# Kernel tuning notes

Measured on AMD Instinct MI355X. Metric: run time of the kernel, lower is better.

## Reference

```python
import jax, jax.numpy as jnp
import numpy as np
from functools import partial

H = 768
E = 1536
B = 4
L = 4096

def layer_norm(x, g, b, eps=1e-5):
    mu = jnp.mean(x, axis=-1, keepdims=True)
    var = jnp.mean((x - mu) ** 2, axis=-1, keepdims=True)
    return (x - mu) * jax.lax.rsqrt(var + eps) * g + b

def l2_normalize(x, eps=1e-12):
    n = jnp.sqrt(jnp.sum(x * x, axis=-1, keepdims=True))
    return x / jnp.maximum(n, eps)

def dw_conv(x, w):
    # x: [B, L, E], w: [E, 1, 3] depthwise kernel (torch Conv1d groups=E layout)
    y = jax.lax.conv_general_dilated(
        x.transpose(0, 2, 1), w, window_strides=(1,), padding=[(1, 1)],
        dimension_numbers=('NCH', 'OIH', 'NCH'), feature_group_count=E)
    return y.transpose(0, 2, 1)

def setup_inputs() -> dict:
    key = jax.random.key(0)
    ks = jax.random.split(key, 12)
    d = {}
    d['x'] = jax.random.normal(ks[0], (B, L, H), jnp.float32)
    d['ln1_g'] = jnp.ones((H,), jnp.float32)
    d['ln1_b'] = jnp.zeros((H,), jnp.float32)
    d['ln2_g'] = jnp.ones((E,), jnp.float32)
    d['ln2_b'] = jnp.zeros((E,), jnp.float32)
    d['W_in'] = 0.02 * jax.random.normal(ks[1], (3 * E, H), jnp.float32)
    d['b_in'] = jnp.zeros((3 * E,), jnp.float32)
    d['W_beta'] = jnp.zeros((E, H), jnp.float32)  # torch init: constant 0
    d['b_beta'] = jnp.ones((E,), jnp.float32)     # torch init: constant 1
    d['W_out'] = 0.02 * jax.random.normal(ks[2], (H, E), jnp.float32)
    d['b_out'] = jnp.zeros((H,), jnp.float32)
    d['W1'] = 0.02 * jax.random.normal(ks[3], (4 * H, H), jnp.float32)
    d['b1'] = jnp.zeros((4 * H,), jnp.float32)
    d['W2'] = 0.02 * jax.random.normal(ks[4], (H, 4 * H), jnp.float32)
    d['b2'] = jnp.zeros((H,), jnp.float32)
    d['conv_w'] = jax.random.normal(ks[5], (E, 1, 3), jnp.float32) / jnp.sqrt(3.0)
    d['attn_scale'] = jnp.ones((1,), jnp.float32)
    return d

def reference(x, ln1_g, ln1_b, ln2_g, ln2_b, W_in, b_in, W_beta, b_beta,
              W_out, b_out, W1, b1, W2, b2, conv_w, attn_scale):
    shortcut = x
    xn = layer_norm(x, ln1_g, ln1_b)
    qkv = xn @ W_in.T + b_in
    q, k, v = jnp.split(qkv, 3, axis=-1)
    q = jax.nn.silu(q)
    k = jax.nn.silu(k)
    v = jax.nn.gelu(v, approximate=False)
    q = l2_normalize(q) + 0.1 * k
    k = l2_normalize(k) + 0.1 * q
    q = dw_conv(q, conv_w)
    k = dw_conv(k, conv_w)
    v = dw_conv(v, conv_w)
    beta = jax.nn.sigmoid(xn @ W_beta.T + b_beta) * 0.9 + 0.1
    # initial state is zero, so v_old = 0 and v_new = beta * v (same math as torch code)
    v_new = beta * v                                   # [B, L, E]
    state = jnp.einsum('ble,blf->bef', v_new, k)       # v_new^T @ k : [B, E, E]
    out = jnp.einsum('blf,bef->ble', q, state)         # q @ state^T
    out = out * attn_scale
    out = layer_norm(out, ln2_g, ln2_b)
    out = out @ W_out.T + b_out
    x = shortcut + out
    h = layer_norm(x, ln1_g, ln1_b)
    h = jax.nn.gelu(h @ W1.T + b1, approximate=False) @ W2.T + b2
    return x + h
```

## Files before the change

### kernel.cpp

```cpp
#include <hip/hip_runtime.h>
#include <hip/hip_bf16.h>
#include <cstdint>
#include <cstddef>

using bf16_t = __hip_bfloat16;
typedef __bf16 bf16x8 __attribute__((ext_vector_type(8)));
typedef __bf16 bf16x4 __attribute__((ext_vector_type(4)));
typedef float f32x4 __attribute__((ext_vector_type(4)));

#define DEVI static __device__ __forceinline__

DEVI float b2f(bf16_t v) { return __bfloat162float(v); }

DEVI float fsigmoid(float x) { return 1.0f / (1.0f + __expf(-x)); }
DEVI float fsilu(float x) { return x * fsigmoid(x); }

DEVI float ferf(float x) {
    const float ax = fabsf(x);
    const float t = 1.0f / fmaf(0.3275911f, ax, 1.0f);
    float p = fmaf(1.061405429f, t, -1.453152027f);
    p = fmaf(p, t, 1.421413741f);
    p = fmaf(p, t, -0.284496736f);
    p = fmaf(p, t, 0.254829592f);
    p = p * t * __expf(-ax * ax);
    return copysignf(1.0f - p, x);
}
DEVI float fgelu(float x) { return 0.5f * x * (1.0f + ferf(x * 0.70710678118654752440f)); }

DEVI void g2l16(const bf16_t* g, bf16_t* l) {
    __builtin_amdgcn_global_load_lds(
        (const __attribute__((address_space(1))) void*)g,
        (__attribute__((address_space(3))) void*)l,
        16, 0, 0);
}

DEVI f32x4 mfma16(bf16x8 a, bf16x8 b, f32x4 c) {
    return __builtin_amdgcn_mfma_f32_16x16x32_bf16(a, b, c, 0, 0, 0);
}

template<int ACT, bool RESID, bool OUTBF, bool QKVSPLIT>
__global__ __launch_bounds__(256) void gemm_nt(
    const bf16_t* __restrict__ A, const bf16_t* __restrict__ B,
    void* __restrict__ Cout, const float* __restrict__ bias,
    const float* __restrict__ resid,
    float* __restrict__ normq, float* __restrict__ normk,
    int M, int N, int K, long long sA, long long sB, long long sC)
{
    __shared__ bf16_t As[128 * 64];
    __shared__ bf16_t Bs[128 * 64];

    const int t  = threadIdx.x;
    const int w  = t >> 6;
    const int ln = t & 63;
    const long long bz = blockIdx.z;
    A += bz * sA;
    B += bz * sB;
    const long long cbase = QKVSPLIT ? 0 : bz * sC;

    const int m0 = blockIdx.y * 128;
    const int n0 = blockIdx.x * 128;
    const int wm = (w >> 1) * 64;
    const int wn = (w & 1) * 64;

    f32x4 acc[4][4] = {};

    const int sr = ln >> 3;
    const int sc = (ln & 7) ^ sr;
    const bf16_t* Ap = A + (size_t)(m0 + w * 32 + sr) * K + sc * 8;
    const bf16_t* Bp = B + (size_t)(n0 + w * 32 + sr) * K + sc * 8;
    bf16_t* ldsA = &As[(w * 32) * 64];
    bf16_t* ldsB = &Bs[(w * 32) * 64];

    const int fr = ln & 15;
    const int qd = ln >> 4;
    int roA[4], roB[4];
#pragma unroll
    for (int i = 0; i < 4; ++i) {
        roA[i] = (wm + i * 16 + fr) * 64;
        roB[i] = (wn + i * 16 + fr) * 64;
    }
    const int so0 = ((qd)     ^ (fr & 7)) * 8;
    const int so1 = ((4 + qd) ^ (fr & 7)) * 8;

    for (int k0 = 0; k0 < K; k0 += 64) {
#pragma unroll
        for (int i = 0; i < 4; ++i) {
            g2l16(Ap + (size_t)(i * 8) * K, ldsA + (i * 8) * 64);
            g2l16(Bp + (size_t)(i * 8) * K, ldsB + (i * 8) * 64);
        }
        Ap += 64; Bp += 64;
        __syncthreads();

        bf16x8 af[4], bfr[4];
#pragma unroll
        for (int i = 0; i < 4; ++i) {
            af[i]  = *(const bf16x8*)&As[roA[i] + so0];
            bfr[i] = *(const bf16x8*)&Bs[roB[i] + so0];
        }
#pragma unroll
        for (int mi = 0; mi < 4; ++mi)
#pragma unroll
            for (int ni = 0; ni < 4; ++ni)
                acc[mi][ni] = mfma16(bfr[ni], af[mi], acc[mi][ni]);
#pragma unroll
        for (int i = 0; i < 4; ++i) {
            af[i]  = *(const bf16x8*)&As[roA[i] + so1];
            bfr[i] = *(const bf16x8*)&Bs[roB[i] + so1];
        }
#pragma unroll
        for (int mi = 0; mi < 4; ++mi)
#pragma unroll
            for (int ni = 0; ni < 4; ++ni)
                acc[mi][ni] = mfma16(bfr[ni], af[mi], acc[mi][ni]);
        __syncthreads();
    }

    const int rb = qd * 4;
    const int seg = QKVSPLIT ? (n0 / 1536) : 0;
    f32x4 bias4[4];
#pragma unroll
    for (int ni = 0; ni < 4; ++ni) {
        f32x4 z = {};
        bias4[ni] = bias ? *(const f32x4*)&bias[n0 + wn + ni * 16 + rb] : z;
    }
#pragma unroll
    for (int mi = 0; mi < 4; ++mi) {
        const int row = m0 + wm + mi * 16 + fr;
        float s2 = 0.f;
#pragma unroll
        for (int ni = 0; ni < 4; ++ni) {
            const int col0 = n0 + wn + ni * 16 + rb;
            f32x4 v = acc[mi][ni] + bias4[ni];
            if constexpr (ACT == 1) {
#pragma unroll
                for (int r = 0; r < 4; ++r) v[r] = fgelu(v[r]);
            }
            if constexpr (ACT == 3) {
                if (seg <= 1) {
#pragma unroll
                    for (int r = 0; r < 4; ++r) v[r] = fsilu(v[r]);
                    s2 += v[0]*v[0] + v[1]*v[1] + v[2]*v[2] + v[3]*v[3];
                } else if (seg == 2) {
#pragma unroll
                    for (int r = 0; r < 4; ++r) v[r] = fgelu(v[r]);
                } else {
#pragma unroll
                    for (int r = 0; r < 4; ++r) v[r] = fsigmoid(v[r]) * 0.9f + 0.1f;
                }
            }
            long long off;
            if constexpr (QKVSPLIT) {
                off = (long long)seg * sC + (long long)row * 1536
                    + (col0 - seg * 1536);
            } else {
                off = cbase + (long long)row * N + col0;
            }
            if constexpr (RESID) v += *(const f32x4*)&resid[off];
            if constexpr (OUTBF) {
                bf16x4 o;
#pragma unroll
                for (int r = 0; r < 4; ++r) o[r] = (__bf16)v[r];
                *(bf16x4*)((bf16_t*)Cout + off) = o;
            } else {
                *(f32x4*)((float*)Cout + off) = v;
            }
        }
        if constexpr (ACT == 3) {
            if (seg <= 1) {
                s2 += __shfl_xor(s2, 16, 64);
                s2 += __shfl_xor(s2, 32, 64);
                if (qd == 0)
                    atomicAdd((seg == 0 ? normq : normk) + row, s2);
            }
        }
    }
}

template<int ACT, bool RESID, bool OUTBF, bool QKVSPLIT>
__global__ __launch_bounds__(512) void gemm256(
    const bf16_t* __restrict__ A, const bf16_t* __restrict__ B,
    void* __restrict__ Cout, const float* __restrict__ bias,
    const float* __restrict__ resid,
    float* __restrict__ normq, float* __restrict__ normk,
    int M, int N, int K, long long sA, long long sB, long long sC)
{
    __shared__ bf16_t As[2][256 * 64];
    __shared__ bf16_t Bs[2][256 * 64];

    const int t  = threadIdx.x;
    const int w  = t >> 6;
    const int ln = t & 63;
    const int wr = w >> 2;
    const int wc = w & 3;
    const long long bz = blockIdx.z;
    A += bz * sA;
    B += bz * sB;
    const long long cbase = QKVSPLIT ? 0 : bz * sC;

    const int m0 = blockIdx.y * 256;
    const int n0 = blockIdx.x * 256;

    const int sr = ln >> 3;
    const int scx = ((ln & 7) ^ sr) * 8;
    const bf16_t* gA[2];
    const bf16_t* gB[2];
    int lA[2], lB[2];
#pragma unroll
    for (int i = 0; i < 2; ++i) {
        const int b  = w * 2 + i;
        const int rA = ((b >> 3) << 7) + ((b & 7) << 3);
        const int rB = ((b >> 2) << 6) + ((b & 3) << 3);
        gA[i] = A + (size_t)(m0 + rA + sr) * K + scx;
        gB[i] = B + (size_t)(n0 + rB + sr) * K + scx;
        lA[i] = rA * 64;
        lB[i] = rB * 64;
    }
    const size_t K64 = (size_t)K * 64;
    const size_t K32 = (size_t)K * 32;
    const int NT = K >> 6;

    const int fr = ln & 15;
    const int qd = ln >> 4;
    const int ck0 = ((qd)     ^ (fr & 7)) * 8;
    const int ck1 = ((4 + qd) ^ (fr & 7)) * 8;
    int roA[8], roB[4];
#pragma unroll
    for (int mi = 0; mi < 8; ++mi) roA[mi] = (wr * 128 + mi * 16 + fr) * 64;
#pragma unroll
    for (int ni = 0; ni < 4; ++ni) roB[ni] = (wc * 64 + ni * 16 + fr) * 64;

    f32x4 acc[8][4] = {};

#define STAGE_A(dst, kc) do { \
    g2l16(gA[0] + (kc),       &(dst)[lA[0]]); \
    g2l16(gA[0] + K64 + (kc), &(dst)[lA[0] + 4096]); \
    g2l16(gA[1] + (kc),       &(dst)[lA[1]]); \
    g2l16(gA[1] + K64 + (kc), &(dst)[lA[1] + 4096]); } while (0)
#define STAGE_B(dst, kc) do { \
    g2l16(gB[0] + (kc),       &(dst)[lB[0]]); \
    g2l16(gB[0] + K32 + (kc), &(dst)[lB[0] + 2048]); \
    g2l16(gB[1] + (kc),       &(dst)[lB[1]]); \
    g2l16(gB[1] + K32 + (kc), &(dst)[lB[1] + 2048]); } while (0)

    STAGE_A(As[0], 0);
    STAGE_B(Bs[0], 0);

    for (int u = 0; u < NT; ++u) {
        const bf16_t* Ac = As[u & 1];
        const bf16_t* Bc = Bs[u & 1];
        bf16_t* An = As[(u + 1) & 1];
        bf16_t* Bn = Bs[(u + 1) & 1];
        const size_t kc1 = (size_t)(u + 1) * 64;
        const bool p1 = (u + 1) < NT;

        if (p1) {
            STAGE_A(An, kc1);
            asm volatile("s_waitcnt vmcnt(4)" ::: "memory");
        } else {
            asm volatile("s_waitcnt vmcnt(0)" ::: "memory");
        }
        __builtin_amdgcn_s_barrier();
        __builtin_amdgcn_sched_barrier(0);
        {
            bf16x8 af[8], bfr[4];
#pragma unroll
            for (int mi = 0; mi < 8; ++mi)
                af[mi] = *(const bf16x8*)&Ac[roA[mi] + ck0];
#pragma unroll
            for (int ni = 0; ni < 4; ++ni)
                bfr[ni] = *(const bf16x8*)&Bc[roB[ni] + ck0];
            __builtin_amdgcn_s_setprio(1);
#pragma unroll
            for (int mi = 0; mi < 8; ++mi)
#pragma unroll
                for (int ni = 0; ni < 4; ++ni)
                    acc[mi][ni] = mfma16(bfr[ni], af[mi], acc[mi][ni]);
            __builtin_amdgcn_s_setprio(0);
        }

        if (p1) STAGE_B(Bn, kc1);
        {
            bf16x8 af[8], bfr[4];
#pragma unroll
            for (int mi = 0; mi < 8; ++mi)
                af[mi] = *(const bf16x8*)&Ac[roA[mi] + ck1];
#pragma unroll
            for (int ni = 0; ni < 4; ++ni)
                bfr[ni] = *(const bf16x8*)&Bc[roB[ni] + ck1];
            __builtin_amdgcn_s_setprio(1);
#pragma unroll
            for (int mi = 0; mi < 8; ++mi)
#pragma unroll
                for (int ni = 0; ni < 4; ++ni)
                    acc[mi][ni] = mfma16(bfr[ni], af[mi], acc[mi][ni]);
            __builtin_amdgcn_s_setprio(0);
        }

        if (p1) {
            asm volatile("s_waitcnt vmcnt(4)" ::: "memory");
            __builtin_amdgcn_s_barrier();
            __builtin_amdgcn_sched_barrier(0);
        }
    }
#undef STAGE_A
#undef STAGE_B

    const int rb = qd * 4;
    const int seg = QKVSPLIT ? (n0 / 1536) : 0;
    f32x4 bias4[4];
#pragma unroll
    for (int ni = 0; ni < 4; ++ni) {
        f32x4 z = {};
        bias4[ni] = bias ? *(const f32x4*)&bias[n0 + wc * 64 + ni * 16 + rb] : z;
    }
#pragma unroll
    for (int mi = 0; mi < 8; ++mi) {
        const int row = m0 + wr * 128 + mi * 16 + fr;
        float s2 = 0.f;
#pragma unroll
        for (int ni = 0; ni < 4; ++ni) {
            const int col0 = n0 + wc * 64 + ni * 16 + rb;
            f32x4 v = acc[mi][ni] + bias4[ni];
            if constexpr (ACT == 1) {
#pragma unroll
                for (int r = 0; r < 4; ++r) v[r] = fgelu(v[r]);
            }
            if constexpr (ACT == 3) {
                if (seg <= 1) {
#pragma unroll
                    for (int r = 0; r < 4; ++r) v[r] = fsilu(v[r]);
                    s2 += v[0]*v[0] + v[1]*v[1] + v[2]*v[2] + v[3]*v[3];
                } else if (seg == 2) {
#pragma unroll
                    for (int r = 0; r < 4; ++r) v[r] = fgelu(v[r]);
                } else {
#pragma unroll
                    for (int r = 0; r < 4; ++r) v[r] = fsigmoid(v[r]) * 0.9f + 0.1f;
                }
            }
            long long off;
            if constexpr (QKVSPLIT) {
                off = (long long)seg * sC + (long long)row * 1536
                    + (col0 - seg * 1536);
            } else {
                off = cbase + (long long)row * N + col0;
            }
            if constexpr (RESID) v += *(const f32x4*)&resid[off];
            if constexpr (OUTBF) {
                bf16x4 o;
#pragma unroll
                for (int r = 0; r < 4; ++r) o[r] = (__bf16)v[r];
                *(bf16x4*)((bf16_t*)Cout + off) = o;
            } else {
                *(f32x4*)((float*)Cout + off) = v;
            }
        }
        if constexpr (ACT == 3) {
            if (seg <= 1) {
                s2 += __shfl_xor(s2, 16, 64);
                s2 += __shfl_xor(s2, 32, 64);
                if (qd == 0)
                    atomicAdd((seg == 0 ? normq : normk) + row, s2);
            }
        }
    }
}

template<int NT>
__global__ __launch_bounds__(NT) void ln_v4(
    const float* __restrict__ x, const float* __restrict__ g,
    const float* __restrict__ b, bf16_t* __restrict__ out)
{
    constexpr int n = NT * 4;
    constexpr int NW = NT / 64;
    const int row = blockIdx.x, t = threadIdx.x;
    f32x4 v = *(const f32x4*)&x[(size_t)row * n + t * 4];
    float s  = v[0] + v[1] + v[2] + v[3];
    float ss = v[0]*v[0] + v[1]*v[1] + v[2]*v[2] + v[3]*v[3];
#pragma unroll
    for (int m = 32; m; m >>= 1) { s += __shfl_xor(s, m, 64); ss += __shfl_xor(ss, m, 64); }
    __shared__ float red[2 * NW];
    const int w = t >> 6;
    if ((t & 63) == 0) { red[w] = s; red[NW + w] = ss; }
    __syncthreads();
    s = 0.f; ss = 0.f;
#pragma unroll
    for (int i = 0; i < NW; ++i) { s += red[i]; ss += red[NW + i]; }
    const float mean = s / n;
    const float rstd = rsqrtf(ss / n - mean * mean + 1e-5f);
    const f32x4 gv = *(const f32x4*)&g[t * 4];
    const f32x4 bv = *(const f32x4*)&b[t * 4];
    bf16x4 o;
#pragma unroll
    for (int r = 0; r < 4; ++r)
        o[r] = (__bf16)((v[r] - mean) * rstd * gv[r] + bv[r]);
    *(bf16x4*)&out[(size_t)row * n + t * 4] = o;
}

__global__ __launch_bounds__(192) void ln_bf16_1536(
    const bf16_t* __restrict__ x, const float* __restrict__ g,
    const float* __restrict__ b, bf16_t* __restrict__ out,
    const float* __restrict__ scale_ptr)
{
    const int row = blockIdx.x, t = threadIdx.x;
    const float scale = scale_ptr[0];
    const bf16x8 x8 = *(const bf16x8*)&x[(size_t)row * 1536 + t * 8];
    float v[8];
    float s = 0.f, ss = 0.f;
#pragma unroll
    for (int i = 0; i < 8; ++i) {
        v[i] = (float)x8[i] * scale;
        s += v[i]; ss += v[i] * v[i];
    }
#pragma unroll
    for (int m = 32; m; m >>= 1) { s += __shfl_xor(s, m, 64); ss += __shfl_xor(ss, m, 64); }
    __shared__ float red[6];
    const int w = t >> 6;
    if ((t & 63) == 0) { red[w] = s; red[3 + w] = ss; }
    __syncthreads();
    s  = red[0] + red[1] + red[2];
    ss = red[3] + red[4] + red[5];
    const float mean = s / 1536.f;
    const float rstd = rsqrtf(ss / 1536.f - mean * mean + 1e-5f);
    const f32x4 g0 = *(const f32x4*)&g[t * 8];
    const f32x4 g1 = *(const f32x4*)&g[t * 8 + 4];
    const f32x4 b0 = *(const f32x4*)&b[t * 8];
    const f32x4 b1 = *(const f32x4*)&b[t * 8 + 4];
    bf16x8 o;
#pragma unroll
    for (int r = 0; r < 4; ++r) {
        o[r]     = (__bf16)((v[r]     - mean) * rstd * g0[r] + b0[r]);
        o[r + 4] = (__bf16)((v[r + 4] - mean) * rstd * g1[r] + b1[r]);
    }
    *(bf16x8*)&out[(size_t)row * 1536 + t * 8] = o;
}

__global__ __launch_bounds__(256) void ac_qk(
    const bf16_t* __restrict__ qs, const bf16_t* __restrict__ ks,
    const float* __restrict__ nq, const float* __restrict__ nk,
    bf16_t* __restrict__ qc, bf16_t* __restrict__ kT,
    const float* __restrict__ cw)
{
    constexpr int L = 4096, E = 1536;
    const int b = blockIdx.z;
    const int e0 = blockIdx.x * 64, l0 = blockIdx.y * 64;
    const int t = threadIdx.x;
    const int e = e0 + (t & 15) * 4;
    const int lbase = l0 + (t >> 4) * 4;
    const size_t rowL = (size_t)b * L;

    float w0[4], w1[4], w2[4];
#pragma unroll
    for (int i = 0; i < 4; ++i) {
        w0[i] = cw[(e + i) * 3 + 0];
        w1[i] = cw[(e + i) * 3 + 1];
        w2[i] = cw[(e + i) * 3 + 2];
    }

    float sq[6][4], sk[6][4];
#pragma unroll
    for (int j = 0; j < 6; ++j) {
        const int l = lbase - 1 + j;
        if (l < 0 || l >= L) {
#pragma unroll
            for (int i = 0; i < 4; ++i) { sq[j][i] = 0.f; sk[j][i] = 0.f; }
            continue;
        }
        const size_t off = (rowL + l) * E + e;
        const bf16x4 q4 = *(const bf16x4*)&qs[off];
        const bf16x4 k4 = *(const bf16x4*)&ks[off];
        const float rq = 1.0f / fmaxf(sqrtf(nq[rowL + l]), 1e-12f);
        const float rk = 1.0f / fmaxf(sqrtf(nk[rowL + l]), 1e-12f);
#pragma unroll
        for (int i = 0; i < 4; ++i) {
            const float q1 = (float)q4[i] * rq + 0.1f * (float)k4[i];
            const float k1 = (float)k4[i] * rk + 0.1f * q1;
            sq[j][i] = q1; sk[j][i] = k1;
        }
    }

#pragma unroll
    for (int j = 0; j < 4; ++j) {
        bf16x4 oq;
#pragma unroll
        for (int i = 0; i < 4; ++i)
            oq[i] = (__bf16)(w0[i] * sq[j][i] + w1[i] * sq[j + 1][i] + w2[i] * sq[j + 2][i]);
        *(bf16x4*)&qc[(rowL + lbase + j) * E + e] = oq;
    }
#pragma unroll
    for (int i = 0; i < 4; ++i) {
        bf16x4 ok;
#pragma unroll
        for (int j = 0; j < 4; ++j)
            ok[j] = (__bf16)(w0[i] * sk[j][i] + w1[i] * sk[j + 1][i] + w2[i] * sk[j + 2][i]);
        *(bf16x4*)&kT[((size_t)b * E + e + i) * L + lbase] = ok;
    }
}

__global__ __launch_bounds__(256) void ac_v(
    const bf16_t* __restrict__ vg, const bf16_t* __restrict__ beta,
    bf16_t* __restrict__ vT, const float* __restrict__ cw)
{
    constexpr int L = 4096, E = 1536;
    const int b = blockIdx.z;
    const int e0 = blockIdx.x * 64, l0 = blockIdx.y * 64;
    const int t = threadIdx.x;
    const int e = e0 + (t & 15) * 4;
    const int lbase = l0 + (t >> 4) * 4;
    const size_t rowL = (size_t)b * L;

    float w0[4], w1[4], w2[4];
#pragma unroll
    for (int i = 0; i < 4; ++i) {
        w0[i] = cw[(e + i) * 3 + 0];
        w1[i] = cw[(e + i) * 3 + 1];
        w2[i] = cw[(e + i) * 3 + 2];
    }

    float s[6][4];
#pragma unroll
    for (int j = 0; j < 6; ++j) {
        const int l = lbase - 1 + j;
        if (l < 0 || l >= L) {
#pragma unroll
            for (int i = 0; i < 4; ++i) s[j][i] = 0.f;
            continue;
        }
        const bf16x4 v4 = *(const bf16x4*)&vg[(rowL + l) * E + e];
#pragma unroll
        for (int i = 0; i < 4; ++i) s[j][i] = (float)v4[i];
    }

    float o[4][4];
#pragma unroll
    for (int j = 0; j < 4; ++j) {
        const bf16x4 b4 = *(const bf16x4*)&beta[(rowL + lbase + j) * E + e];
#pragma unroll
        for (int i = 0; i < 4; ++i)
            o[j][i] = (w0[i] * s[j][i] + w1[i] * s[j + 1][i] + w2[i] * s[j + 2][i])
                      * (float)b4[i];
    }
#pragma unroll
    for (int i = 0; i < 4; ++i) {
        bf16x4 ov;
#pragma unroll
        for (int j = 0; j < 4; ++j) ov[j] = (__bf16)o[j][i];
        *(bf16x4*)&vT[((size_t)b * E + e + i) * L + lbase] = ov;
    }
}

__global__ __launch_bounds__(256) void prep1(
    const float* __restrict__ Win, const float* __restrict__ Wbeta,
    const float* __restrict__ bin, const float* __restrict__ bbeta,
    bf16_t* __restrict__ Wcat, float* __restrict__ bcat)
{
    constexpr int nWin4 = 3 * 1536 * 768 / 4;
    constexpr int nWb4  = 1536 * 768 / 4;
    const int i = blockIdx.x * 256 + threadIdx.x;
    if (i < nWin4) {
        const f32x4 v = ((const f32x4*)Win)[i];
        bf16x4 o;
#pragma unroll
        for (int r = 0; r < 4; ++r) o[r] = (__bf16)v[r];
        ((bf16x4*)Wcat)[i] = o;
    } else if (i < nWin4 + nWb4) {
        const f32x4 v = ((const f32x4*)Wbeta)[i - nWin4];
        bf16x4 o;
#pragma unroll
        for (int r = 0; r < 4; ++r) o[r] = (__bf16)v[r];
        ((bf16x4*)Wcat)[i] = o;
    } else {
        const int j = i - nWin4 - nWb4;
        ((f32x4*)bcat)[j] = (j < 1152) ? ((const f32x4*)bin)[j]
                                       : ((const f32x4*)bbeta)[j - 1152];
    }
}

__global__ __launch_bounds__(256) void prep2(
    const float* __restrict__ Wout, const float* __restrict__ W1,
    const float* __restrict__ W2, bf16_t* __restrict__ dst)
{
    constexpr int n0 = 768 * 1536 / 4;
    constexpr int n1 = n0 + 3072 * 768 / 4;
    const int i = blockIdx.x * 256 + threadIdx.x;
    const float* src;
    int j;
    if (i < n0)      { src = Wout; j = i; }
    else if (i < n1) { src = W1;   j = i - n0; }
    else             { src = W2;   j = i - n1; }
    const f32x4 v = ((const f32x4*)src)[j];
    bf16x4 o;
#pragma unroll
    for (int r = 0; r < 4; ++r) o[r] = (__bf16)v[r];
    ((bf16x4*)dst)[i] = o;
}

__global__ void diag_ws(float* o, float v) { o[threadIdx.x] = v; }


extern "C" void kernel_launch(void* const* d_in, const int* in_sizes, int n_in,
                              void* d_out, int out_size, void* d_ws, size_t ws_size,
                              hipStream_t stream)
{
    constexpr int B = 4, L = 4096, H = 768, E = 1536;
    constexpr int T = B * L;
    constexpr size_t SEGE = (size_t)T * E;
    constexpr size_t S    = SEGE * 2;
    constexpr size_t o_bcat  = 5 * S;
    constexpr size_t o_norms = o_bcat + 6144 * 4;
    constexpr size_t WS_NEED = o_norms + (size_t)T * 8;

    const float* x       = (const float*)d_in[0];
    const float* ln1_g   = (const float*)d_in[1];
    const float* ln1_b   = (const float*)d_in[2];
    const float* ln2_g   = (const float*)d_in[3];
    const float* ln2_b   = (const float*)d_in[4];
    const float* W_in    = (const float*)d_in[5];
    const float* b_in    = (const float*)d_in[6];
    const float* W_beta  = (const float*)d_in[7];
    const float* b_beta  = (const float*)d_in[8];
    const float* W_out   = (const float*)d_in[9];
    const float* b_out   = (const float*)d_in[10];
    const float* W1      = (const float*)d_in[11];
    const float* b1      = (const float*)d_in[12];
    const float* W2      = (const float*)d_in[13];
    const float* b2      = (const float*)d_in[14];
    const float* conv_w  = (const float*)d_in[15];
    const float* attn_sc = (const float*)d_in[16];

    if (ws_size < WS_NEED) {
        diag_ws<<<1, 256, 0, stream>>>((float*)d_out,
                                       10000.0f + (float)(ws_size >> 20));
        return;
    }

    char* ws = (char*)d_ws;
    bf16_t* slotA = (bf16_t*)(ws + 0 * S);
    bf16_t* slotB = (bf16_t*)(ws + 1 * S);
    bf16_t* slotC = (bf16_t*)(ws + 2 * S);
    bf16_t* slotD = (bf16_t*)(ws + 3 * S);
    bf16_t* slotE = (bf16_t*)(ws + 4 * S);
    float*  bcat  = (float*)(ws + o_bcat);
    float*  nq    = (float*)(ws + o_norms);
    float*  nk    = nq + T;

    bf16_t* Wcat = slotE;
    bf16_t* xn   = (bf16_t*)((char*)slotE + (size_t)6144 * H * 2);

    bf16_t* vT    = slotE;
    bf16_t* kT    = slotC;
    bf16_t* qc    = slotD;
    bf16_t* state = slotA;
    bf16_t* WoutB = (bf16_t*)((char*)slotA + (size_t)20 * 1024 * 1024);
    bf16_t* W1B   = WoutB + (size_t)H * E;
    bf16_t* W2B   = W1B + (size_t)4 * H * H;
    bf16_t* attn  = slotB;
    bf16_t* ln2o  = slotE;
    float*  x2    = (float*)slotC;
    bf16_t* xn2   = slotB;
    bf16_t* h1    = slotD;

    hipMemsetAsync(nq, 0, (size_t)T * 2 * sizeof(float), stream);
    prep1<<<4614, 256, 0, stream>>>(W_in, W_beta, b_in, b_beta, Wcat, bcat);

    ln_v4<192><<<T, 192, 0, stream>>>(x, ln1_g, ln1_b, xn);

    gemm256<3, false, true, true><<<dim3(6144 / 256, T / 256, 1), 512, 0, stream>>>(
        xn, Wcat, slotA, bcat, nullptr, nq, nk, T, 6144, H, 0, 0, (long long)SEGE);

    ac_v <<<dim3(E / 64, L / 64, B), 256, 0, stream>>>(slotC, slotD, vT, conv_w);
    ac_qk<<<dim3(E / 64, L / 64, B), 256, 0, stream>>>(slotA, slotB, nq, nk, qc, kT, conv_w);

    prep2<<<5760, 256, 0, stream>>>(W_out, W1, W2, WoutB);

    gemm_nt<0, false, true, false><<<dim3(E / 128, E / 128, B), 256, 0, stream>>>(
        vT, kT, state, nullptr, nullptr, nullptr, nullptr, E, E, L,
        (long long)E * L, (long long)E * L, (long long)E * E);

    gemm256<0, false, true, false><<<dim3(E / 256, L / 256, B), 512, 0, stream>>>(
        qc, state, attn, nullptr, nullptr, nullptr, nullptr, L, E, E,
        (long long)L * E, (long long)E * E, (long long)L * E);

    ln_bf16_1536<<<T, 192, 0, stream>>>(attn, ln2_g, ln2_b, ln2o, attn_sc);

    gemm_nt<0, true, false, false><<<dim3(H / 128, T / 128, 1), 256, 0, stream>>>(
        ln2o, WoutB, x2, b_out, x, nullptr, nullptr, T, H, E, 0, 0, 0);

    ln_v4<192><<<T, 192, 0, stream>>>(x2, ln1_g, ln1_b, xn2);

    gemm256<1, false, true, false><<<dim3(4 * H / 256, T / 256, 1), 512, 0, stream>>>(
        xn2, W1B, h1, b1, nullptr, nullptr, nullptr, T, 4 * H, H, 0, 0, 0);

    gemm_nt<0, true, false, false><<<dim3(H / 128, T / 128, 1), 256, 0, stream>>>(
        h1, W2B, (float*)d_out, b2, x2, nullptr, nullptr, T, H, 4 * H, 0, 0, 0);
}
```

Before: 1.013 ms.

## Double-buffer LDS tiles in gemm_nt and drop setprio in second GEMM

The 128x128 gemm_nt kernel now keeps two LDS buffers and prefetches the next K tile's A and B with global_load_lds while computing the current one. It uses explicit vmcnt waits and raw barriers, the same scheme the other GEMM kernel already uses. This is meant to hide global-load latency behind the MFMA work. LDS use per block doubles to 64 KB, which may reduce occupancy. The s_setprio raises around the MFMA loops in the other GEMM are also removed.

```diff
diff --git a/kernel.cpp b/kernel.cpp
--- a/kernel.cpp
+++ b/kernel.cpp
@@ -46,8 +46,8 @@
     float* __restrict__ normq, float* __restrict__ normk,
     int M, int N, int K, long long sA, long long sB, long long sC)
 {
-    __shared__ bf16_t As[128 * 64];
-    __shared__ bf16_t Bs[128 * 64];
+    __shared__ bf16_t As[2][128 * 64];
+    __shared__ bf16_t Bs[2][128 * 64];
 
     const int t  = threadIdx.x;
     const int w  = t >> 6;
@@ -68,8 +68,7 @@
     const int sc = (ln & 7) ^ sr;
     const bf16_t* Ap = A + (size_t)(m0 + w * 32 + sr) * K + sc * 8;
     const bf16_t* Bp = B + (size_t)(n0 + w * 32 + sr) * K + sc * 8;
-    bf16_t* ldsA = &As[(w * 32) * 64];
-    bf16_t* ldsB = &Bs[(w * 32) * 64];
+    const int lw = (w * 32) * 64;
 
     const int fr = ln & 15;
     const int qd = ln >> 4;
@@ -82,38 +81,77 @@
     const int so0 = ((qd)     ^ (fr & 7)) * 8;
     const int so1 = ((4 + qd) ^ (fr & 7)) * 8;
 
-    for (int k0 = 0; k0 < K; k0 += 64) {
-#pragma unroll
-        for (int i = 0; i < 4; ++i) {
-            g2l16(Ap + (size_t)(i * 8) * K, ldsA + (i * 8) * 64);
-            g2l16(Bp + (size_t)(i * 8) * K, ldsB + (i * 8) * 64);
-        }
-        Ap += 64; Bp += 64;
-        __syncthreads();
-
-        bf16x8 af[4], bfr[4];
-#pragma unroll
-        for (int i = 0; i < 4; ++i) {
-            af[i]  = *(const bf16x8*)&As[roA[i] + so0];
-            bfr[i] = *(const bf16x8*)&Bs[roB[i] + so0];
-        }
-#pragma unroll
-        for (int mi = 0; mi < 4; ++mi)
-#pragma unroll
-            for (int ni = 0; ni < 4; ++ni)
-                acc[mi][ni] = mfma16(bfr[ni], af[mi], acc[mi][ni]);
-#pragma unroll
-        for (int i = 0; i < 4; ++i) {
-            af[i]  = *(const bf16x8*)&As[roA[i] + so1];
-            bfr[i] = *(const bf16x8*)&Bs[roB[i] + so1];
-        }
-#pragma unroll
-        for (int mi = 0; mi < 4; ++mi)
-#pragma unroll
-            for (int ni = 0; ni < 4; ++ni)
-                acc[mi][ni] = mfma16(bfr[ni], af[mi], acc[mi][ni]);
-        __syncthreads();
-    }
+    const int NT = K >> 6;
+
+#define STAGE_A(nb, kc) do { \
+    bf16_t* d_ = &As[nb][lw]; \
+    g2l16(Ap + (kc),                  d_); \
+    g2l16(Ap + (size_t)( 8) * K + (kc), d_ +  8 * 64); \
+    g2l16(Ap + (size_t)(16) * K + (kc), d_ + 16 * 64); \
+    g2l16(Ap + (size_t)(24) * K + (kc), d_ + 24 * 64); } while (0)
+#define STAGE_B(nb, kc) do { \
+    bf16_t* d_ = &Bs[nb][lw]; \
+    g2l16(Bp + (kc),                  d_); \
+    g2l16(Bp + (size_t)( 8) * K + (kc), d_ +  8 * 64); \
+    g2l16(Bp + (size_t)(16) * K + (kc), d_ + 16 * 64); \
+    g2l16(Bp + (size_t)(24) * K + (kc), d_ + 24 * 64); } while (0)
+
+    STAGE_A(0, 0);
+    STAGE_B(0, 0);
+
+    for (int u = 0; u < NT; ++u) {
+        const int cb = u & 1;
+        const int nb = cb ^ 1;
+        const bf16_t* Ac = As[cb];
+        const bf16_t* Bc = Bs[cb];
+        const size_t kc1 = (size_t)(u + 1) * 64;
+        const bool p1 = (u + 1) < NT;
+
+        if (p1) {
+            STAGE_A(nb, kc1);
+            asm volatile("s_waitcnt vmcnt(4)" ::: "memory");
+        } else {
+            asm volatile("s_waitcnt vmcnt(0)" ::: "memory");
+        }
+        __builtin_amdgcn_s_barrier();
+        __builtin_amdgcn_sched_barrier(0);
+        {
+            bf16x8 af[4], bfr[4];
+#pragma unroll
+            for (int i = 0; i < 4; ++i) {
+                af[i]  = *(const bf16x8*)&Ac[roA[i] + so0];
+                bfr[i] = *(const bf16x8*)&Bc[roB[i] + so0];
+            }
+#pragma unroll
+            for (int mi = 0; mi < 4; ++mi)
+#pragma unroll
+                for (int ni = 0; ni < 4; ++ni)
+                    acc[mi][ni] = mfma16(bfr[ni], af[mi], acc[mi][ni]);
+        }
+
+        if (p1) STAGE_B(nb, kc1);
+        {
+            bf16x8 af[4], bfr[4];
+#pragma unroll
+            for (int i = 0; i < 4; ++i) {
+                af[i]  = *(const bf16x8*)&Ac[roA[i] + so1];
+                bfr[i] = *(const bf16x8*)&Bc[roB[i] + so1];
+            }
+#pragma unroll
+            for (int mi = 0; mi < 4; ++mi)
+#pragma unroll
+                for (int ni = 0; ni < 4; ++ni)
+                    acc[mi][ni] = mfma16(bfr[ni], af[mi], acc[mi][ni]);
+        }
+
+        if (p1) {
+            asm volatile("s_waitcnt vmcnt(4)" ::: "memory");
+            __builtin_amdgcn_s_barrier();
+            __builtin_amdgcn_sched_barrier(0);
+        }
+    }
+#undef STAGE_A
+#undef STAGE_B
 
     const int rb = qd * 4;
     const int seg = QKVSPLIT ? (n0 / 1536) : 0;
@@ -269,13 +307,11 @@
 #pragma unroll
             for (int ni = 0; ni < 4; ++ni)
                 bfr[ni] = *(const bf16x8*)&Bc[roB[ni] + ck0];
-            __builtin_amdgcn_s_setprio(1);
 #pragma unroll
             for (int mi = 0; mi < 8; ++mi)
 #pragma unroll
                 for (int ni = 0; ni < 4; ++ni)
                     acc[mi][ni] = mfma16(bfr[ni], af[mi], acc[mi][ni]);
-            __builtin_amdgcn_s_setprio(0);
         }
 
         if (p1) STAGE_B(Bn, kc1);
@@ -287,13 +323,11 @@
 #pragma unroll
             for (int ni = 0; ni < 4; ++ni)
                 bfr[ni] = *(const bf16x8*)&Bc[roB[ni] + ck1];
-            __builtin_amdgcn_s_setprio(1);
 #pragma unroll
             for (int mi = 0; mi < 8; ++mi)
 #pragma unroll
                 for (int ni = 0; ni < 4; ++ni)
                     acc[mi][ni] = mfma16(bfr[ni], af[mi], acc[mi][ni]);
-            __builtin_amdgcn_s_setprio(0);
         }
 
         if (p1) {
```

After: 1.238 ms. 1.22x slower.
